# Kernel tuning notes

Measured on AMD Instinct MI355X. Metric: run time of the kernel, lower is better.

## Reference

```python
import jax, jax.numpy as jnp
import numpy as np
from jax.scipy.linalg import solve_triangular

OMEGA = 1.5  # params_fix['omega']
BS, N, MAXITER = 512, 256, 200
RTOL = 1e-6


def setup_inputs() -> dict:
    key = jax.random.key(0)
    k1, k2, k3 = jax.random.split(key, 3)
    # diagonally dominant A so SOR converges
    A = jax.random.normal(k1, (BS, N, N), jnp.float32) + N * jnp.eye(N, dtype=jnp.float32)
    b = jax.random.normal(k2, (BS, N), jnp.float32)
    x_sol = jnp.linalg.solve(A, b[..., None])[..., 0]
    theta = jax.random.normal(k3, (BS, N), jnp.float32)  # initial iterate x0
    rtol = jnp.full((BS,), RTOL, jnp.float32)
    return {"A": A, "b": b, "x_sol": x_sol, "theta": theta, "rtol": rtol, "maxiter": MAXITER}


def reference(A, b, x_sol, theta, rtol, maxiter):
    bs, n, _ = A.shape
    b = b.reshape(bs, n, 1)
    x0 = theta.reshape(bs, n, 1)
    xs = x_sol.reshape(bs, n, 1)

    diag = jnp.diagonal(A, axis1=1, axis2=2)          # [bs, n]
    D = jnp.eye(n, dtype=A.dtype) * diag[:, :, None]  # diag_embed
    L = jnp.tril(A, -1)
    U = jnp.triu(A, 1)

    omega = jnp.asarray(OMEGA, A.dtype)
    G1 = D + omega * L                      # lower triangular, [bs, n, n]
    G2 = omega * U + (omega - 1.0) * D
    G = solve_triangular(G1, -G2, lower=True)        # iteration matrix
    f = solve_triangular(G1, omega * b, lower=True)  # affine term

    err0 = jnp.linalg.norm(xs - x0, axis=(1, 2))     # [bs]
    xtol = jnp.linalg.norm(xs, axis=(1, 2)) * rtol   # [bs]

    def step(carry, _):
        x, err, done = carry
        # global stopping criterion: while any(err > xtol)
        done = jnp.logical_or(done, jnp.logical_not(jnp.any(err > xtol)))
        x_new = jnp.where(done, x, G @ x + f)
        err_new = jnp.where(done, err, jnp.linalg.norm(xs - x_new, axis=(1, 2)))
        hist = jnp.where(done, jnp.zeros_like(err), err_new)  # unwritten slots stay 0
        return (x_new, err_new, done), hist

    init = (x0, err0, jnp.asarray(False))
    _, hist = jax.lax.scan(step, init, None, length=maxiter)  # hist: [maxiter, bs]
    return jnp.concatenate([err0[:, None], hist.T], axis=1)   # [bs, maxiter+1]
```

## Files before the change

kernel.cpp:

```cpp
#include <hip/hip_runtime.h>
#include <math.h>

#define BS 512
#define NN 256
#define RB 16
#define OMEGA_F 1.5f


__global__ __launch_bounds__(512)
void sor_gmat(const float* __restrict__ A, float* __restrict__ gws)
{
    const int bp  = blockIdx.x;
    const int b   = bp >> 1;
    const int p   = bp & 1;
    const int tid = threadIdx.x;
    const int tc  = tid & 127;
    const int t   = 128 * p + tc;
    const int q   = tid >> 7;
    const int qU  = __builtin_amdgcn_readfirstlane(q);
    const float* __restrict__ Ab = A + (size_t)b * NN * NN;

    __shared__ __align__(16) char smem[49152];
    float (*ldsA)[NN]       = (float (*)[NN])(smem);
    float (*acc2)[RB][128]  = (float (*)[RB][128])(smem + 16384);
    float (*xbuf)[128]      = (float (*)[128])(smem + 16384);
    float (*ldsT)[128]      = (float (*)[128])(smem);

    float g[4][RB];
    for (int KB = 0; KB < NN / RB; ++KB) {
        const int r0 = KB * RB;
        __syncthreads();
        #pragma unroll
        for (int i = 0; i < 2; ++i) {
            const int lin = tid + 512 * i;
            const int rr = lin >> 6, c4 = (lin & 63) << 2;
            *(float4*)&ldsA[rr][c4] = *(const float4*)&Ab[(size_t)(r0 + rr) * NN + c4];
        }
        __syncthreads();

        float acc[RB];
        #pragma unroll
        for (int rr = 0; rr < RB; ++rr) acc[rr] = 0.f;
        #pragma unroll
        for (int m = 0; m < 4; ++m) {
            const int kb = 4 * m + qU;
            if (kb < KB) {
                const int j0 = kb * RB;
                #pragma unroll
                for (int jw = 0; jw < 4; ++jw) {
                    const float g0 = g[m][4 * jw + 0];
                    const float g1 = g[m][4 * jw + 1];
                    const float g2 = g[m][4 * jw + 2];
                    const float g3 = g[m][4 * jw + 3];
                    #pragma unroll
                    for (int hc = 0; hc < 4; ++hc) {
                        float4 a_[4];
                        #pragma unroll
                        for (int h = 0; h < 4; ++h)
                            a_[h] = *(const float4*)&ldsA[4 * hc + h][j0 + 4 * jw];
                        #pragma unroll
                        for (int h = 0; h < 4; ++h)
                            acc[4 * hc + h] += a_[h].x * g0 + a_[h].y * g1
                                             + a_[h].z * g2 + a_[h].w * g3;
                    }
                }
            }
        }
        if (q >= 1) {
            #pragma unroll
            for (int rr = 0; rr < RB; ++rr) acc2[q - 1][rr][tc] = acc[rr];
        }
        __syncthreads();
        if (q == 0) {
            float s_[RB];
            #pragma unroll
            for (int rr = 0; rr < RB; ++rr)
                s_[rr] = acc[rr] + acc2[0][rr][tc] + acc2[1][rr][tc] + acc2[2][rr][tc];
            #pragma unroll
            for (int rr = 0; rr < RB; ++rr) {
                const int r = r0 + rr;
                const float a_rt = ldsA[rr][t];
                const float brt  = (t > r) ? (-OMEGA_F) * a_rt
                                 : ((t == r) ? (1.0f - OMEGA_F) * a_rt : 0.0f);
                const float diag = ldsA[rr][r];
                const float val  = (brt - OMEGA_F * s_[rr]) / diag;
                xbuf[rr][tc] = val;
                #pragma unroll
                for (int rr2 = rr + 1; rr2 < RB; ++rr2)
                    s_[rr2] += ldsA[rr2][r] * val;
            }
        }
        __syncthreads();
        #pragma unroll
        for (int m = 0; m < 4; ++m) {
            if (KB == 4 * m + q) {
                #pragma unroll
                for (int rr = 0; rr < RB; ++rr) g[m][rr] = xbuf[rr][tc];
            }
        }
    }

    const int u8 = tid & 63, wl = tid >> 6;
    float* __restrict__ gb = gws + (size_t)b * (NN * NN);
    #pragma unroll
    for (int R = 0; R < 4; ++R) {
        __syncthreads();
        #pragma unroll
        for (int rr = 0; rr < RB; ++rr) {
            const int lr = q * RB + rr;
            ldsT[lr][(tc + 4 * lr) & 127] = g[R][rr];
        }
        __syncthreads();
        #pragma unroll
        for (int k = 0; k < 4; ++k) {
            const int cl = 16 * wl + 4 * k;
            const float4 v = *(const float4*)&ldsT[u8][(cl + 4 * u8) & 127];
            *(float4*)&gb[((size_t)((R * 4 + k) * 16 + 8 * p + wl)) * 256 + 4 * u8] = v;
        }
    }
}

__global__ __launch_bounds__(1024)
void sor_iter(const float* __restrict__ gws,
              const float* __restrict__ xs,
              const float* __restrict__ x0,
              const float* __restrict__ rtol,
              const int* __restrict__ maxiter_p,
              float* __restrict__ out)
{
    const int b   = blockIdx.x;
    const int tid = threadIdx.x;
    const int w   = __builtin_amdgcn_readfirstlane(tid >> 6);
    const int u   = tid & 63;

    __shared__ __align__(16) char smem[148544];
    float* gl            = (float*)smem;
    float* e             = (float*)(smem + 131072);
    float (*pbuf)[4][64] = (float (*)[4][64])(smem + 132096);
    float* nrm           = (float*)(smem + 148480);
    float* rs            = (float*)(smem + 148496);

    const int mi = *maxiter_p;
    float* __restrict__ outb = out + (size_t)b * (mi + 1);
    const float* __restrict__ gb = gws + (size_t)b * (NN * NN);

    if (tid < NN) {
        const float xsv = xs[b * NN + tid];
        const float ev  = xsv - x0[b * NN + tid];
        e[tid] = ev;
        float s1 = ev * ev, s2 = xsv * xsv;
        #pragma unroll
        for (int off = 32; off > 0; off >>= 1) {
            s1 += __shfl_down(s1, off);
            s2 += __shfl_down(s2, off);
        }
        if (u == 0) { rs[tid >> 6] = s1; rs[4 + (tid >> 6)] = s2; }
    }

    float4 gi[2][4];
    #pragma unroll
    for (int rg = 0; rg < 2; ++rg)
        #pragma unroll
        for (int k = 0; k < 4; ++k)
            gi[rg][k] = *(const float4*)&gb[(size_t)((rg * 4 + k) * 16 + w) * 256 + 4 * u];
    #pragma unroll
    for (int rg = 0; rg < 2; ++rg)
        #pragma unroll
        for (int k = 0; k < 4; ++k) {
            const float4 v = *(const float4*)&gb[(size_t)(((rg + 2) * 4 + k) * 16 + w) * 256 + 4 * u];
            *(float4*)&gl[((rg * 4 + k) * 16 + w) * 256 + 4 * u] = v;
        }
    __syncthreads();
    const float err0 = sqrtf(rs[0] + rs[1] + rs[2] + rs[3]);
    const float xtol = sqrtf(rs[4] + rs[5] + rs[6] + rs[7]) * rtol[b];
    if (tid == 0) outb[0] = err0;

    const float4* __restrict__ e4 = (const float4*)e;
    float err = err0;
    int s = 1;
    for (; s <= mi; ++s) {
        if (!(err > xtol)) break;
        float a0 = 0.f, a1 = 0.f, a2 = 0.f, a3 = 0.f;
        #pragma unroll
        for (int k = 0; k < 4; ++k) {
            const float4 ev4 = e4[4 * w + k];
            const float4 v2 = *(const float4*)&gl[(k * 16 + w) * 256 + 4 * u];
            const float4 v3 = *(const float4*)&gl[((4 + k) * 16 + w) * 256 + 4 * u];
            a0 += gi[0][k].x*ev4.x + gi[0][k].y*ev4.y + gi[0][k].z*ev4.z + gi[0][k].w*ev4.w;
            a1 += gi[1][k].x*ev4.x + gi[1][k].y*ev4.y + gi[1][k].z*ev4.z + gi[1][k].w*ev4.w;
            a2 += v2.x*ev4.x + v2.y*ev4.y + v2.z*ev4.z + v2.w*ev4.w;
            a3 += v3.x*ev4.x + v3.y*ev4.y + v3.z*ev4.z + v3.w*ev4.w;
        }
        pbuf[w][0][u] = a0;
        pbuf[w][1][u] = a1;
        pbuf[w][2][u] = a2;
        pbuf[w][3][u] = a3;
        __syncthreads();
        if (tid < NN) {
            const int kk = tid >> 6, uu = tid & 63;
            float sum = 0.f;
            #pragma unroll
            for (int w2 = 0; w2 < 16; ++w2) sum += pbuf[w2][kk][uu];
            e[tid] = sum;
            float loc = sum * sum;
            #pragma unroll
            for (int off = 32; off > 0; off >>= 1) loc += __shfl_down(loc, off);
            if (uu == 0) nrm[kk] = loc;
        }
        __syncthreads();
        err = sqrtf(nrm[0] + nrm[1] + nrm[2] + nrm[3]);
        if (tid == 0) outb[s] = err;
    }
    for (int idx = s + tid; idx <= mi; idx += 1024) outb[idx] = 0.f;
}

extern "C" void kernel_launch(void* const* d_in, const int* in_sizes, int n_in,
                              void* d_out, int out_size, void* d_ws, size_t ws_size,
                              hipStream_t stream) {
    const float* A     = (const float*)d_in[0];
    const float* xs    = (const float*)d_in[2];
    const float* theta = (const float*)d_in[3];
    const float* rtol  = (const float*)d_in[4];
    const int*   mi    = (const int*)d_in[5];
    float* out = (float*)d_out;
    float* gws = (float*)d_ws;

    sor_gmat<<<dim3(BS * 2), dim3(512), 0, stream>>>(A, gws);
    sor_iter<<<dim3(BS), dim3(1024), 0, stream>>>(gws, xs, theta, rtol, mi, out);
}
```

Measured before the change: 655.4 us.

## Keep full solved column block in LDS and stream A rows from global

The gmat kernel now stores all solved rows of its 128-column slice of G in a 128KB LDS buffer instead of per-thread registers. It loads only its own 128 columns of A plus a 16x16 diagonal tile into LDS, and reads the off-diagonal A values for the update directly from global memory as wave-uniform loads. The cross-wave reduction becomes a two-level tree. The final transposed write reads straight from LDS, which removes the per-iteration register distribution step and the transpose staging. The cost is much larger LDS use (about 153KB), which limits occupancy to one block per CU, and more global/scalar-cache traffic for A.

```diff
diff --git a/kernel.cpp b/kernel.cpp
--- a/kernel.cpp
+++ b/kernel.cpp
@@ -20,21 +20,22 @@
     const int qU  = __builtin_amdgcn_readfirstlane(q);
     const float* __restrict__ Ab = A + (size_t)b * NN * NN;
 
-    __shared__ __align__(16) char smem[49152];
-    float (*ldsA)[NN]       = (float (*)[NN])(smem);
-    float (*acc2)[RB][128]  = (float (*)[RB][128])(smem + 16384);
-    float (*xbuf)[128]      = (float (*)[128])(smem + 16384);
-    float (*ldsT)[128]      = (float (*)[128])(smem);
-
-    float g[4][RB];
+    __shared__ __align__(16) char smem[156672];
+    float* Xl              = (float*)smem;
+    float (*ldsA)[128]     = (float (*)[128])(smem + 131072);
+    float (*ldsD)[16]      = (float (*)[16])(smem + 139264);
+    float (*acc2)[RB][128] = (float (*)[RB][128])(smem + 140288);
+
     for (int KB = 0; KB < NN / RB; ++KB) {
         const int r0 = KB * RB;
         __syncthreads();
-        #pragma unroll
-        for (int i = 0; i < 2; ++i) {
-            const int lin = tid + 512 * i;
-            const int rr = lin >> 6, c4 = (lin & 63) << 2;
-            *(float4*)&ldsA[rr][c4] = *(const float4*)&Ab[(size_t)(r0 + rr) * NN + c4];
+        {
+            const int rr = tid >> 5, c4 = (tid & 31) << 2;
+            *(float4*)&ldsA[rr][c4] = *(const float4*)&Ab[(size_t)(r0 + rr) * NN + 128 * p + c4];
+        }
+        if (tid < 64) {
+            const int rr = tid >> 2, c4 = (tid & 3) << 2;
+            *(float4*)&ldsD[rr][c4] = *(const float4*)&Ab[(size_t)(r0 + rr) * NN + r0 + c4];
         }
         __syncthreads();
 
@@ -46,76 +47,69 @@
             const int kb = 4 * m + qU;
             if (kb < KB) {
                 const int j0 = kb * RB;
+                float xv[RB];
                 #pragma unroll
-                for (int jw = 0; jw < 4; ++jw) {
-                    const float g0 = g[m][4 * jw + 0];
-                    const float g1 = g[m][4 * jw + 1];
-                    const float g2 = g[m][4 * jw + 2];
-                    const float g3 = g[m][4 * jw + 3];
+                for (int jj = 0; jj < RB; ++jj)
+                    xv[jj] = Xl[(j0 + jj) * 128 + tc];
+                #pragma unroll
+                for (int rr = 0; rr < RB; ++rr) {
                     #pragma unroll
-                    for (int hc = 0; hc < 4; ++hc) {
-                        float4 a_[4];
-                        #pragma unroll
-                        for (int h = 0; h < 4; ++h)
-                            a_[h] = *(const float4*)&ldsA[4 * hc + h][j0 + 4 * jw];
-                        #pragma unroll
-                        for (int h = 0; h < 4; ++h)
-                            acc[4 * hc + h] += a_[h].x * g0 + a_[h].y * g1
-                                             + a_[h].z * g2 + a_[h].w * g3;
+                    for (int j4 = 0; j4 < 4; ++j4) {
+                        const float4 av = *(const float4*)&Ab[(size_t)(r0 + rr) * NN + j0 + 4 * j4];
+                        acc[rr] += av.x * xv[4 * j4 + 0] + av.y * xv[4 * j4 + 1]
+                                 + av.z * xv[4 * j4 + 2] + av.w * xv[4 * j4 + 3];
                     }
                 }
             }
         }
-        if (q >= 1) {
-            #pragma unroll
-            for (int rr = 0; rr < RB; ++rr) acc2[q - 1][rr][tc] = acc[rr];
+        if (q >= 2) {
+            #pragma unroll
+            for (int rr = 0; rr < RB; ++rr) acc2[q - 2][rr][tc] = acc[rr];
+        }
+        __syncthreads();
+        if (q == 1) {
+            #pragma unroll
+            for (int rr = 0; rr < RB; ++rr) {
+                acc[rr] += acc2[1][rr][tc];
+                acc2[1][rr][tc] = acc[rr];
+            }
+        }
+        if (q == 0) {
+            #pragma unroll
+            for (int rr = 0; rr < RB; ++rr) acc[rr] += acc2[0][rr][tc];
         }
         __syncthreads();
         if (q == 0) {
             float s_[RB];
             #pragma unroll
-            for (int rr = 0; rr < RB; ++rr)
-                s_[rr] = acc[rr] + acc2[0][rr][tc] + acc2[1][rr][tc] + acc2[2][rr][tc];
+            for (int rr = 0; rr < RB; ++rr) s_[rr] = acc[rr] + acc2[1][rr][tc];
             #pragma unroll
             for (int rr = 0; rr < RB; ++rr) {
                 const int r = r0 + rr;
-                const float a_rt = ldsA[rr][t];
+                const float a_rt = ldsA[rr][tc];
                 const float brt  = (t > r) ? (-OMEGA_F) * a_rt
                                  : ((t == r) ? (1.0f - OMEGA_F) * a_rt : 0.0f);
-                const float diag = ldsA[rr][r];
+                const float diag = ldsD[rr][rr];
                 const float val  = (brt - OMEGA_F * s_[rr]) / diag;
-                xbuf[rr][tc] = val;
+                Xl[r * 128 + tc] = val;
                 #pragma unroll
                 for (int rr2 = rr + 1; rr2 < RB; ++rr2)
-                    s_[rr2] += ldsA[rr2][r] * val;
+                    s_[rr2] += ldsD[rr2][rr] * val;
             }
         }
-        __syncthreads();
-        #pragma unroll
-        for (int m = 0; m < 4; ++m) {
-            if (KB == 4 * m + q) {
-                #pragma unroll
-                for (int rr = 0; rr < RB; ++rr) g[m][rr] = xbuf[rr][tc];
-            }
-        }
-    }
+    }
+    __syncthreads();
 
     const int u8 = tid & 63, wl = tid >> 6;
     float* __restrict__ gb = gws + (size_t)b * (NN * NN);
     #pragma unroll
-    for (int R = 0; R < 4; ++R) {
-        __syncthreads();
-        #pragma unroll
-        for (int rr = 0; rr < RB; ++rr) {
-            const int lr = q * RB + rr;
-            ldsT[lr][(tc + 4 * lr) & 127] = g[R][rr];
-        }
-        __syncthreads();
+    for (int rg = 0; rg < 4; ++rg) {
+        const int row = 64 * rg + u8;
         #pragma unroll
         for (int k = 0; k < 4; ++k) {
             const int cl = 16 * wl + 4 * k;
-            const float4 v = *(const float4*)&ldsT[u8][(cl + 4 * u8) & 127];
-            *(float4*)&gb[((size_t)((R * 4 + k) * 16 + 8 * p + wl)) * 256 + 4 * u8] = v;
+            const float4 v = *(const float4*)&Xl[row * 128 + cl];
+            *(float4*)&gb[((size_t)((rg * 4 + k) * 16 + 8 * p + wl)) * 256 + 4 * u8] = v;
         }
     }
 }
```

Result: slower. 769.0 us (+17.3%).
